# Kernel tuning notes

Measured on AMD Instinct MI355X. Metric: run time of the kernel, lower is better.

Reference implementation:

```python
import jax, jax.numpy as jnp
import numpy as np

N_NODES = 50000
N_EDGES = 800000
NFEAT, NHID, NCLASS = 512, 256, 128
N_UV = 2048


def gcn_layer(x, adj_row, adj_col, adj_val, W, b):
    # support = x @ W ; out = A @ support (sparse COO spmm) + b
    support = x @ W                                   # [N, out]
    msgs = adj_val[:, None] * support[adj_col]        # [E, out]
    out = jax.ops.segment_sum(msgs, adj_row, num_segments=N_NODES)
    return out + b


def setup_inputs() -> dict:
    key = jax.random.key(0)
    ks = jax.random.split(key, 12)
    u = jax.random.randint(ks[0], (N_UV,), 0, N_NODES)
    v = jax.random.randint(ks[1], (N_UV,), 0, N_NODES)
    x = jax.random.normal(ks[2], (N_NODES, NFEAT), dtype=jnp.float32)
    adj_row = jnp.sort(jax.random.randint(ks[3], (N_EDGES,), 0, N_NODES))
    adj_col = jax.random.randint(ks[4], (N_EDGES,), 0, N_NODES)
    adj_val = jax.random.uniform(ks[5], (N_EDGES,), dtype=jnp.float32)
    s1 = 1.0 / np.sqrt(NHID)
    s2 = 1.0 / np.sqrt(NCLASS)
    W1 = jax.random.uniform(ks[6], (NFEAT, NHID), minval=-s1, maxval=s1, dtype=jnp.float32)
    b1 = jax.random.uniform(ks[7], (NHID,), minval=-s1, maxval=s1, dtype=jnp.float32)
    W2 = jax.random.uniform(ks[8], (NHID, NCLASS), minval=-s2, maxval=s2, dtype=jnp.float32)
    b2 = jax.random.uniform(ks[9], (NCLASS,), minval=-s2, maxval=s2, dtype=jnp.float32)
    We = jax.random.normal(ks[10], (NCLASS, NCLASS), dtype=jnp.float32) * (1.0 / np.sqrt(NCLASS))
    return {"u": u, "v": v, "x": x, "adj_row": adj_row, "adj_col": adj_col,
            "adj_val": adj_val, "W1": W1, "b1": b1, "W2": W2, "b2": b2, "We": We}


def reference(u, v, x, adj_row, adj_col, adj_val, W1, b1, W2, b2, We):
    # layer 1: GCN + ReLU (dropout is identity in eval mode)
    h = jax.nn.relu(gcn_layer(x, adj_row, adj_col, adj_val, W1, b1))
    # layer 2: GCN
    z = gcn_layer(h, adj_row, adj_col, adj_val, W2, b2)          # [N, nclass]
    # edge scoring: sigmoid(w_edge(z[u]) @ z[v].T)
    zu = z[u] @ We.T                                             # [U, nclass] (nn.Linear: x @ W.T)
    zv = z[v]                                                    # [V, nclass]
    p_uv = jax.nn.sigmoid(zu @ zv.T)                             # [U, V]
    return p_uv
```

## Files before the change

### kernel.cpp

```cpp
#include <hip/hip_runtime.h>
#include <hip/hip_bf16.h>
#include <math.h>

#define N_NODES 50000
#define N_EDGES 800000
#define NFEAT   512
#define NHID    256
#define NCLASS  128
#define N_UV    2048

#define Q24_SCALE  524288.0f
#define Q24_INV    1.9073486328125e-6f

typedef __bf16    bf16x8 __attribute__((ext_vector_type(8)));
typedef short     s16x8  __attribute__((ext_vector_type(8)));
typedef float     f32x4  __attribute__((ext_vector_type(4)));

struct __attribute__((packed)) U3 { unsigned a, b, c; };

__device__ __forceinline__ unsigned short bf16_rn(float f) {
  unsigned u = __float_as_uint(f);
  u += 0x7fffu + ((u >> 16) & 1u);
  return (unsigned short)(u >> 16);
}
__device__ __forceinline__ float bf16_to_f(unsigned short h) {
  return __uint_as_float(((unsigned)h) << 16);
}
__device__ __forceinline__ void unpack24(unsigned a, unsigned b, unsigned c,
                                         int& e0, int& e1, int& e2, int& e3) {
  e0 = ((int)(a << 8)) >> 8;
  e1 = ((int)((b << 16) | ((a >> 24) << 8))) >> 8;
  e2 = ((int)((c << 24) | ((b >> 16) << 8))) >> 8;
  e3 = ((int)c) >> 8;
}

#define LDSPAD 72

template <bool ASPLIT, int OMODE>
__global__ __launch_bounds__(256, 4) void gemm_mfma_wide(
    const float* __restrict__ Af,
    const unsigned short* __restrict__ Ahi, const unsigned short* __restrict__ Alo,
    const unsigned short* __restrict__ BThi, const unsigned short* __restrict__ BTlo,
    float* __restrict__ C, unsigned char* __restrict__ Cq,
    const float* __restrict__ bias, int M, int N, int K) {
  __shared__ unsigned short sAh[2][64 * LDSPAD];
  __shared__ unsigned short sAl[2][64 * LDSPAD];

  const int tid  = threadIdx.x;
  const int lane = tid & 63;
  const int wave = tid >> 6;
  const int wn   = wave << 5;
  const int lm   = lane & 15;
  const int quad = lane >> 4;
  const int m0   = blockIdx.y * 64;
  const int n0   = blockIdx.x * 128;

  const int r32 = tid >> 4;
  const int c32 = (tid & 15) * 4;
  const int r16 = tid >> 3;
  const int c16 = (tid & 7) * 8;

  float4 pA[4]; s16x8 pAh[2], pAl[2];

  f32x4 acc[4][2];
#pragma unroll
  for (int i = 0; i < 4; ++i)
#pragma unroll
    for (int j = 0; j < 2; ++j)
#pragma unroll
      for (int r = 0; r < 4; ++r) acc[i][j][r] = 0.f;

#define LOAD_TILE(k0)                                                          \
  do {                                                                         \
    if (ASPLIT) {                                                              \
      _Pragma("unroll") for (int p = 0; p < 4; ++p) {                          \
        const int m = m0 + p * 16 + r32;                                       \
        pA[p] = make_float4(0.f, 0.f, 0.f, 0.f);                               \
        if (m < M) pA[p] = *(const float4*)&Af[(size_t)m * K + (k0) + c32];    \
      }                                                                        \
    } else {                                                                   \
      _Pragma("unroll") for (int p = 0; p < 2; ++p) {                          \
        const int m = m0 + p * 32 + r16;                                       \
        _Pragma("unroll") for (int e = 0; e < 8; ++e) { pAh[p][e] = 0; pAl[p][e] = 0; } \
        if (m < M) {                                                           \
          pAh[p] = *(const s16x8*)&Ahi[(size_t)m * K + (k0) + c16];            \
          pAl[p] = *(const s16x8*)&Alo[(size_t)m * K + (k0) + c16];            \
        }                                                                      \
      }                                                                        \
    }                                                                          \
  } while (0)

#define SPLIT4W(v, hv, lv)                                                     \
  hv.x = bf16_rn(v.x); lv.x = bf16_rn(v.x - bf16_to_f(hv.x));                  \
  hv.y = bf16_rn(v.y); lv.y = bf16_rn(v.y - bf16_to_f(hv.y));                  \
  hv.z = bf16_rn(v.z); lv.z = bf16_rn(v.z - bf16_to_f(hv.z));                  \
  hv.w = bf16_rn(v.w); lv.w = bf16_rn(v.w - bf16_to_f(hv.w));

#define STORE_TILE(buf)                                                        \
  do {                                                                         \
    if (ASPLIT) {                                                              \
      _Pragma("unroll") for (int p = 0; p < 4; ++p) {                          \
        ushort4 hv, lv; SPLIT4W(pA[p], hv, lv);                                \
        const int row = p * 16 + r32;                                          \
        *(ushort4*)&sAh[buf][row * LDSPAD + c32] = hv;                         \
        *(ushort4*)&sAl[buf][row * LDSPAD + c32] = lv;                         \
      }                                                                        \
    } else {                                                                   \
      _Pragma("unroll") for (int p = 0; p < 2; ++p) {                          \
        const int row = p * 32 + r16;                                          \
        *(s16x8*)&sAh[buf][row * LDSPAD + c16] = pAh[p];                       \
        *(s16x8*)&sAl[buf][row * LDSPAD + c16] = pAl[p];                       \
      }                                                                        \
    }                                                                          \
  } while (0)

  LOAD_TILE(0);
  STORE_TILE(0);

  const unsigned short* Bhrow = BThi + (size_t)(n0 + wn + lm) * K;
  const unsigned short* Blrow = BTlo + (size_t)(n0 + wn + lm) * K;

  __syncthreads();

  const int NT = K >> 6;
  for (int t = 0; t < NT; ++t) {
    const int k0  = t << 6;
    const int cur = t & 1;
    const unsigned short* bufh = &sAh[cur][0];
    const unsigned short* bufl = &sAl[cur][0];

    bf16x8 bH[2][2], bL[2][2];
#pragma unroll
    for (int ks = 0; ks < 2; ++ks)
#pragma unroll
      for (int j = 0; j < 2; ++j) {
        const size_t off = (size_t)(j * 16) * K + k0 + ks * 32 + quad * 8;
        bH[ks][j] = __builtin_bit_cast(bf16x8, *(const s16x8*)(Bhrow + off));
        bL[ks][j] = __builtin_bit_cast(bf16x8, *(const s16x8*)(Blrow + off));
      }

    if (t + 1 < NT) LOAD_TILE(k0 + 64);

#pragma unroll
    for (int ks = 0; ks < 2; ++ks) {
      const int koff = ks * 32 + quad * 8;
#pragma unroll
      for (int i = 0; i < 4; ++i) {
        const int r = i * 16 + lm;
        const bf16x8 aH = __builtin_bit_cast(bf16x8, *(const s16x8*)&bufh[r * LDSPAD + koff]);
        const bf16x8 aL = __builtin_bit_cast(bf16x8, *(const s16x8*)&bufl[r * LDSPAD + koff]);
#pragma unroll
        for (int j = 0; j < 2; ++j) {
          acc[i][j] = __builtin_amdgcn_mfma_f32_16x16x32_bf16(aH, bH[ks][j], acc[i][j], 0, 0, 0);
          acc[i][j] = __builtin_amdgcn_mfma_f32_16x16x32_bf16(aH, bL[ks][j], acc[i][j], 0, 0, 0);
          acc[i][j] = __builtin_amdgcn_mfma_f32_16x16x32_bf16(aL, bH[ks][j], acc[i][j], 0, 0, 0);
        }
      }
    }

    if (t + 1 < NT) STORE_TILE(cur ^ 1);
    __syncthreads();
  }

#pragma unroll
  for (int i = 0; i < 4; ++i)
#pragma unroll
    for (int j = 0; j < 2; ++j) {
      const int col = n0 + wn + j * 16 + lm;
      const float bb = (OMODE == 3) ? bias[col] : 0.f;
#pragma unroll
      for (int r = 0; r < 4; ++r) {
        const int row = m0 + i * 16 + quad * 4 + r;
        if (row < M) {
          float v = acc[i][j][r];
          if (OMODE == 2) {
            int q = __float2int_rn(v * Q24_SCALE);
            q = q > 8388607 ? 8388607 : (q < -8388608 ? -8388608 : q);
            unsigned char* p = Cq + ((size_t)row * N + col) * 3;
            p[0] = (unsigned char)(q & 0xFF);
            p[1] = (unsigned char)((q >> 8) & 0xFF);
            p[2] = (unsigned char)((q >> 16) & 0xFF);
          } else if (OMODE == 3) {
            C[(size_t)row * N + col] = v + bb;
          } else {
            C[(size_t)row * N + col] = v;
          }
        }
      }
    }
#undef LOAD_TILE
#undef STORE_TILE
#undef SPLIT4W
}

template <int OMODE>
__global__ __launch_bounds__(256, 2) void gemm_mfma_split(
    const float* __restrict__ Af, const float* __restrict__ BTf,
    float* __restrict__ C, int M, int N, int K) {
  __shared__ unsigned short sAh[128 * LDSPAD];
  __shared__ unsigned short sAl[128 * LDSPAD];
  __shared__ unsigned short sBh[128 * LDSPAD];
  __shared__ unsigned short sBl[128 * LDSPAD];

  const int tid  = threadIdx.x;
  const int lane = tid & 63;
  const int wave = tid >> 6;
  const int wm   = (wave >> 1) << 6;
  const int wn   = (wave & 1) << 6;
  const int lm   = lane & 15;
  const int quad = lane >> 4;
  const int m0   = blockIdx.y * 128;
  const int n0   = blockIdx.x * 128;

  const int r32 = tid >> 4;
  const int c32 = (tid & 15) * 4;

  float4 pA[8];
  float4 pB[8];

  f32x4 acc[4][4];
#pragma unroll
  for (int i = 0; i < 4; ++i)
#pragma unroll
    for (int j = 0; j < 4; ++j)
#pragma unroll
      for (int r = 0; r < 4; ++r) acc[i][j][r] = 0.f;

#define LOAD_TILE(k0)                                                          \
  do {                                                                         \
    _Pragma("unroll") for (int p = 0; p < 8; ++p) {                            \
      const int m = m0 + p * 16 + r32;                                         \
      pA[p] = make_float4(0.f, 0.f, 0.f, 0.f);                                 \
      if (m < M) pA[p] = *(const float4*)&Af[(size_t)m * K + (k0) + c32];      \
    }                                                                          \
    _Pragma("unroll") for (int p = 0; p < 8; ++p) {                            \
      const int n = n0 + p * 16 + r32;                                         \
      pB[p] = *(const float4*)&BTf[(size_t)n * K + (k0) + c32];                \
    }                                                                          \
  } while (0)

#define SPLIT4(v, hv, lv)                                                      \
  hv.x = bf16_rn(v.x); lv.x = bf16_rn(v.x - bf16_to_f(hv.x));                  \
  hv.y = bf16_rn(v.y); lv.y = bf16_rn(v.y - bf16_to_f(hv.y));                  \
  hv.z = bf16_rn(v.z); lv.z = bf16_rn(v.z - bf16_to_f(hv.z));                  \
  hv.w = bf16_rn(v.w); lv.w = bf16_rn(v.w - bf16_to_f(hv.w));

#define STORE_TILE()                                                           \
  do {                                                                         \
    _Pragma("unroll") for (int p = 0; p < 8; ++p) {                            \
      ushort4 hv, lv; SPLIT4(pA[p], hv, lv);                                   \
      const int row = p * 16 + r32;                                            \
      *(ushort4*)&sAh[row * LDSPAD + c32] = hv;                                \
      *(ushort4*)&sAl[row * LDSPAD + c32] = lv;                                \
    }                                                                          \
    _Pragma("unroll") for (int p = 0; p < 8; ++p) {                            \
      ushort4 hv, lv; SPLIT4(pB[p], hv, lv);                                   \
      const int row = p * 16 + r32;                                            \
      *(ushort4*)&sBh[row * LDSPAD + c32] = hv;                                \
      *(ushort4*)&sBl[row * LDSPAD + c32] = lv;                                \
    }                                                                          \
  } while (0)

  LOAD_TILE(0);

  for (int k0 = 0; k0 < K; k0 += 64) {
    if (k0) __syncthreads();
    STORE_TILE();
    __syncthreads();
    if (k0 + 64 < K) LOAD_TILE(k0 + 64);

#pragma unroll
    for (int ks = 0; ks < 2; ++ks) {
      const int koff = ks * 32 + quad * 8;
      bf16x8 aH[4], aL[4], bH[4], bL[4];
#pragma unroll
      for (int i = 0; i < 4; ++i) {
        const int r = wm + i * 16 + lm;
        aH[i] = __builtin_bit_cast(bf16x8, *(const s16x8*)&sAh[r * LDSPAD + koff]);
        aL[i] = __builtin_bit_cast(bf16x8, *(const s16x8*)&sAl[r * LDSPAD + koff]);
      }
#pragma unroll
      for (int j = 0; j < 4; ++j) {
        const int r = wn + j * 16 + lm;
        bH[j] = __builtin_bit_cast(bf16x8, *(const s16x8*)&sBh[r * LDSPAD + koff]);
        bL[j] = __builtin_bit_cast(bf16x8, *(const s16x8*)&sBl[r * LDSPAD + koff]);
      }
#pragma unroll
      for (int i = 0; i < 4; ++i)
#pragma unroll
        for (int j = 0; j < 4; ++j) {
          acc[i][j] = __builtin_amdgcn_mfma_f32_16x16x32_bf16(aH[i], bH[j], acc[i][j], 0, 0, 0);
          acc[i][j] = __builtin_amdgcn_mfma_f32_16x16x32_bf16(aH[i], bL[j], acc[i][j], 0, 0, 0);
          acc[i][j] = __builtin_amdgcn_mfma_f32_16x16x32_bf16(aL[i], bH[j], acc[i][j], 0, 0, 0);
        }
    }
  }

#pragma unroll
  for (int i = 0; i < 4; ++i)
#pragma unroll
    for (int j = 0; j < 4; ++j) {
      const int col = n0 + wn + j * 16 + lm;
#pragma unroll
      for (int r = 0; r < 4; ++r) {
        const int row = m0 + wm + i * 16 + quad * 4 + r;
        if (row < M) {
          float v = acc[i][j][r];
          if (OMODE == 1) v = 1.f / (1.f + expf(-v));
          C[(size_t)row * N + col] = v;
        }
      }
    }
#undef LOAD_TILE
#undef STORE_TILE
#undef SPLIT4
}

__global__ __launch_bounds__(256) void prep_all(
    const int* __restrict__ rows, int* __restrict__ row_ptr,
    const float* __restrict__ W1, unsigned short* __restrict__ W1Thi,
    unsigned short* __restrict__ W1Tlo,
    const float* __restrict__ W2, unsigned short* __restrict__ W2Thi,
    unsigned short* __restrict__ W2Tlo) {
  const int idx = blockIdx.x * 256 + threadIdx.x;
  if (idx < N_EDGES) {
    const int r = rows[idx];
    const int rprev = (idx == 0) ? -1 : rows[idx - 1];
    for (int n = rprev + 1; n <= r; ++n) row_ptr[n] = idx;
    if (idx == N_EDGES - 1)
      for (int n = r + 1; n <= N_NODES; ++n) row_ptr[n] = N_EDGES;
  }
  if (idx < NFEAT * NHID) {
    const int n = idx / NFEAT;
    const int k = idx - n * NFEAT;
    const float f = W1[(size_t)k * NHID + n];
    const unsigned short h = bf16_rn(f);
    W1Thi[idx] = h;
    W1Tlo[idx] = bf16_rn(f - bf16_to_f(h));
  }
  if (idx < NHID * NCLASS) {
    const int n = idx / NHID;
    const int k = idx - n * NHID;
    const float f = W2[(size_t)k * NCLASS + n];
    const unsigned short h = bf16_rn(f);
    W2Thi[idx] = h;
    W2Tlo[idx] = bf16_rn(f - bf16_to_f(h));
  }
}

__global__ __launch_bounds__(256, 4) void spmm256_q24_f32(
    const unsigned char* __restrict__ Sq, const int* __restrict__ row_ptr,
    const int* __restrict__ cols, const float* __restrict__ vals,
    const float4* __restrict__ bias4, float4* __restrict__ outF) {
  const int wave = threadIdx.x >> 6;
  const int lane = threadIdx.x & 63;
  const int node = blockIdx.x * 4 + wave;

  const int lou = __builtin_amdgcn_readfirstlane(row_ptr[node]);
  const int hiu = __builtin_amdgcn_readfirstlane(row_ptr[node + 1]);

  float4 acc = make_float4(0.f, 0.f, 0.f, 0.f);
  const int lane12 = lane * 12;

  for (int base = lou; base < hiu; base += 16) {
    int   c[16];
    float w[16];
    if (base + 16 <= hiu) {
#pragma unroll
      for (int t = 0; t < 16; ++t) {
        c[t] = cols[base + t];
        w[t] = vals[base + t] * Q24_INV;
      }
    } else {
#pragma unroll
      for (int t = 0; t < 16; ++t) {
        const int idx = base + t;
        const int ide = idx < hiu ? idx : hiu - 1;
        c[t] = cols[ide];
        w[t] = idx < hiu ? vals[ide] * Q24_INV : 0.f;
      }
    }
    U3 d[16];
#pragma unroll
    for (int t = 0; t < 16; ++t)
      d[t] = *(const U3*)&Sq[(size_t)c[t] * (NHID * 3) + lane12];
#pragma unroll
    for (int t = 0; t < 16; ++t) {
      int e0, e1, e2, e3;
      unpack24(d[t].a, d[t].b, d[t].c, e0, e1, e2, e3);
      acc.x = fmaf(w[t], (float)e0, acc.x);
      acc.y = fmaf(w[t], (float)e1, acc.y);
      acc.z = fmaf(w[t], (float)e2, acc.z);
      acc.w = fmaf(w[t], (float)e3, acc.w);
    }
  }

  const float4 b = bias4[lane];
  acc.x = fmaxf(acc.x + b.x, 0.f);
  acc.y = fmaxf(acc.y + b.y, 0.f);
  acc.z = fmaxf(acc.z + b.z, 0.f);
  acc.w = fmaxf(acc.w + b.w, 0.f);

  outF[(size_t)node * 64 + lane] = acc;
}

__global__ __launch_bounds__(256, 4) void spmm256_f32_list(
    const float4* __restrict__ H4, const int* __restrict__ row_ptr,
    const int* __restrict__ cols, const float* __restrict__ vals,
    const int* __restrict__ u, const int* __restrict__ v,
    float4* __restrict__ out4) {
  const int wave = threadIdx.x >> 6;
  const int lane = threadIdx.x & 63;
  const int idx  = blockIdx.x * 4 + wave;
  const int node = idx < N_UV ? u[idx] : v[idx - N_UV];

  const int lou = __builtin_amdgcn_readfirstlane(row_ptr[node]);
  const int hiu = __builtin_amdgcn_readfirstlane(row_ptr[node + 1]);

  float4 acc = make_float4(0.f, 0.f, 0.f, 0.f);

  for (int base = lou; base < hiu; base += 16) {
    int   c[16];
    float w[16];
    if (base + 16 <= hiu) {
#pragma unroll
      for (int t = 0; t < 16; ++t) { c[t] = cols[base + t]; w[t] = vals[base + t]; }
    } else {
#pragma unroll
      for (int t = 0; t < 16; ++t) {
        const int e = base + t;
        const int ie = e < hiu ? e : hiu - 1;
        c[t] = cols[ie];
        w[t] = e < hiu ? vals[ie] : 0.f;
      }
    }
    float4 r[16];
#pragma unroll
    for (int t = 0; t < 16; ++t) r[t] = H4[(size_t)c[t] * 64 + lane];
#pragma unroll
    for (int t = 0; t < 16; ++t) {
      acc.x = fmaf(w[t], r[t].x, acc.x); acc.y = fmaf(w[t], r[t].y, acc.y);
      acc.z = fmaf(w[t], r[t].z, acc.z); acc.w = fmaf(w[t], r[t].w, acc.w);
    }
  }

  out4[(size_t)idx * 64 + lane] = acc;
}

extern "C" void kernel_launch(void* const* d_in, const int* in_sizes, int n_in,
                              void* d_out, int out_size, void* d_ws, size_t ws_size,
                              hipStream_t stream) {
  const int*   u       = (const int*)  d_in[0];
  const int*   v       = (const int*)  d_in[1];
  const float* x       = (const float*)d_in[2];
  const int*   adj_row = (const int*)  d_in[3];
  const int*   adj_col = (const int*)  d_in[4];
  const float* adj_val = (const float*)d_in[5];
  const float* W1      = (const float*)d_in[6];
  const float* b1      = (const float*)d_in[7];
  const float* W2      = (const float*)d_in[8];
  const float* b2      = (const float*)d_in[9];
  const float* We      = (const float*)d_in[10];
  float* out = (float*)d_out;

  char* wsb = (char*)d_ws;
  unsigned char* S1q = (unsigned char*)wsb;
  float* ZUV2 = (float*)wsb;
  float* ZUV  = (float*)(wsb + (4u << 20));
  float* ZU   = (float*)(wsb + (6u << 20));
  float* Hf = (float*)(wsb + (size_t)N_NODES * NHID * sizeof(float));
  unsigned short* W1Thi = (unsigned short*)out;
  unsigned short* W1Tlo = W1Thi + NHID * NFEAT;
  unsigned short* W2Thi = W1Tlo + NHID * NFEAT;
  unsigned short* W2Tlo = W2Thi + NCLASS * NHID;
  int* row_ptr = (int*)(W2Tlo + NCLASS * NHID);

  prep_all<<<(N_EDGES + 255) / 256, 256, 0, stream>>>(
      adj_row, row_ptr, W1, W1Thi, W1Tlo, W2, W2Thi, W2Tlo);

  gemm_mfma_wide<true, 2>
      <<<dim3(NHID / 128, (N_NODES + 63) / 64), 256, 0, stream>>>(
      x, nullptr, nullptr, W1Thi, W1Tlo,
      nullptr, S1q, nullptr, N_NODES, NHID, NFEAT);

  spmm256_q24_f32<<<N_NODES / 4, 256, 0, stream>>>(
      S1q, row_ptr, adj_col, adj_val, (const float4*)b1, (float4*)Hf);

  spmm256_f32_list<<<(2 * N_UV) / 4, 256, 0, stream>>>(
      (const float4*)Hf, row_ptr, adj_col, adj_val, u, v, (float4*)ZUV2);

  gemm_mfma_wide<true, 3>
      <<<dim3(NCLASS / 128, (2 * N_UV) / 64), 256, 0, stream>>>(
      ZUV2, nullptr, nullptr, W2Thi, W2Tlo,
      ZUV, nullptr, b2, 2 * N_UV, NCLASS, NHID);

  gemm_mfma_split<0>
      <<<dim3(NCLASS / 128, N_UV / 128), 256, 0, stream>>>(
      ZUV, We, ZU, N_UV, NCLASS, NCLASS);

  gemm_mfma_split<1>
      <<<dim3(N_UV / 128, N_UV / 128), 256, 0, stream>>>(
      ZU, ZUV + (size_t)N_UV * NCLASS, out, N_UV, N_UV, NCLASS);
}
```

Baseline: 365.2 us.

## Fold edge weight We into W2 and pre-split zv to drop two GEMM launches

Precomputes W2·We^T and b2·We^T in a small prep kernel, so the u-half of the layer-2 GEMM directly yields z[u]@We^T while the v-half uses plain W2. The v-half output is written pre-split into bf16 hi/lo, which lets the final scoring GEMM reuse the wide kernel with sigmoid epilogue instead of the split-on-the-fly kernel. This removes the separate We GEMM and the in-loop conversion of B in the final GEMM. It adds a prep launch and changes the rounding order of the We product, which slightly alters numerics.

```diff
diff --git a/kernel.cpp b/kernel.cpp
--- a/kernel.cpp
+++ b/kernel.cpp
@@ -41,8 +41,11 @@
     const float* __restrict__ Af,
     const unsigned short* __restrict__ Ahi, const unsigned short* __restrict__ Alo,
     const unsigned short* __restrict__ BThi, const unsigned short* __restrict__ BTlo,
+    const unsigned short* __restrict__ BThi2, const unsigned short* __restrict__ BTlo2,
     float* __restrict__ C, unsigned char* __restrict__ Cq,
-    const float* __restrict__ bias, int M, int N, int K) {
+    unsigned short* __restrict__ Chi, unsigned short* __restrict__ Clo,
+    const float* __restrict__ bias, const float* __restrict__ bias2,
+    int M, int N, int K) {
   __shared__ unsigned short sAh[2][64 * LDSPAD];
   __shared__ unsigned short sAl[2][64 * LDSPAD];
 
@@ -54,6 +57,11 @@
   const int quad = lane >> 4;
   const int m0   = blockIdx.y * 64;
   const int n0   = blockIdx.x * 128;
+
+  const bool vh = (OMODE == 5) && ((int)blockIdx.y >= (M >> 7));
+  const unsigned short* selBh = (OMODE == 5 && vh) ? BThi2 : BThi;
+  const unsigned short* selBl = (OMODE == 5 && vh) ? BTlo2 : BTlo;
+  const float*          selBi = (OMODE == 5 && vh) ? bias2 : bias;
 
   const int r32 = tid >> 4;
   const int c32 = (tid & 15) * 4;
@@ -117,8 +125,8 @@
   LOAD_TILE(0);
   STORE_TILE(0);
 
-  const unsigned short* Bhrow = BThi + (size_t)(n0 + wn + lm) * K;
-  const unsigned short* Blrow = BTlo + (size_t)(n0 + wn + lm) * K;
+  const unsigned short* Bhrow = selBh + (size_t)(n0 + wn + lm) * K;
+  const unsigned short* Blrow = selBl + (size_t)(n0 + wn + lm) * K;
 
   __syncthreads();
 
@@ -167,7 +175,7 @@
 #pragma unroll
     for (int j = 0; j < 2; ++j) {
       const int col = n0 + wn + j * 16 + lm;
-      const float bb = (OMODE == 3) ? bias[col] : 0.f;
+      const float bb = (OMODE == 3 || OMODE == 5) ? selBi[col] : 0.f;
 #pragma unroll
       for (int r = 0; r < 4; ++r) {
         const int row = m0 + i * 16 + quad * 4 + r;
@@ -180,8 +188,20 @@
             p[0] = (unsigned char)(q & 0xFF);
             p[1] = (unsigned char)((q >> 8) & 0xFF);
             p[2] = (unsigned char)((q >> 16) & 0xFF);
+          } else if (OMODE == 1) {
+            C[(size_t)row * N + col] = 1.f / (1.f + expf(-v));
           } else if (OMODE == 3) {
             C[(size_t)row * N + col] = v + bb;
+          } else if (OMODE == 5) {
+            v += bb;
+            if (!vh) {
+              C[(size_t)row * N + col] = v;
+            } else {
+              const unsigned short h = bf16_rn(v);
+              const size_t o = (size_t)(row - (M >> 1)) * N + col;
+              Chi[o] = h;
+              Clo[o] = bf16_rn(v - bf16_to_f(h));
+            }
           } else {
             C[(size_t)row * N + col] = v;
           }
@@ -191,129 +211,6 @@
 #undef LOAD_TILE
 #undef STORE_TILE
 #undef SPLIT4W
-}
-
-template <int OMODE>
-__global__ __launch_bounds__(256, 2) void gemm_mfma_split(
-    const float* __restrict__ Af, const float* __restrict__ BTf,
-    float* __restrict__ C, int M, int N, int K) {
-  __shared__ unsigned short sAh[128 * LDSPAD];
-  __shared__ unsigned short sAl[128 * LDSPAD];
-  __shared__ unsigned short sBh[128 * LDSPAD];
-  __shared__ unsigned short sBl[128 * LDSPAD];
-
-  const int tid  = threadIdx.x;
-  const int lane = tid & 63;
-  const int wave = tid >> 6;
-  const int wm   = (wave >> 1) << 6;
-  const int wn   = (wave & 1) << 6;
-  const int lm   = lane & 15;
-  const int quad = lane >> 4;
-  const int m0   = blockIdx.y * 128;
-  const int n0   = blockIdx.x * 128;
-
-  const int r32 = tid >> 4;
-  const int c32 = (tid & 15) * 4;
-
-  float4 pA[8];
-  float4 pB[8];
-
-  f32x4 acc[4][4];
-#pragma unroll
-  for (int i = 0; i < 4; ++i)
-#pragma unroll
-    for (int j = 0; j < 4; ++j)
-#pragma unroll
-      for (int r = 0; r < 4; ++r) acc[i][j][r] = 0.f;
-
-#define LOAD_TILE(k0)                                                          \
-  do {                                                                         \
-    _Pragma("unroll") for (int p = 0; p < 8; ++p) {                            \
-      const int m = m0 + p * 16 + r32;                                         \
-      pA[p] = make_float4(0.f, 0.f, 0.f, 0.f);                                 \
-      if (m < M) pA[p] = *(const float4*)&Af[(size_t)m * K + (k0) + c32];      \
-    }                                                                          \
-    _Pragma("unroll") for (int p = 0; p < 8; ++p) {                            \
-      const int n = n0 + p * 16 + r32;                                         \
-      pB[p] = *(const float4*)&BTf[(size_t)n * K + (k0) + c32];                \
-    }                                                                          \
-  } while (0)
-
-#define SPLIT4(v, hv, lv)                                                      \
-  hv.x = bf16_rn(v.x); lv.x = bf16_rn(v.x - bf16_to_f(hv.x));                  \
-  hv.y = bf16_rn(v.y); lv.y = bf16_rn(v.y - bf16_to_f(hv.y));                  \
-  hv.z = bf16_rn(v.z); lv.z = bf16_rn(v.z - bf16_to_f(hv.z));                  \
-  hv.w = bf16_rn(v.w); lv.w = bf16_rn(v.w - bf16_to_f(hv.w));
-
-#define STORE_TILE()                                                           \
-  do {                                                                         \
-    _Pragma("unroll") for (int p = 0; p < 8; ++p) {                            \
-      ushort4 hv, lv; SPLIT4(pA[p], hv, lv);                                   \
-      const int row = p * 16 + r32;                                            \
-      *(ushort4*)&sAh[row * LDSPAD + c32] = hv;                                \
-      *(ushort4*)&sAl[row * LDSPAD + c32] = lv;                                \
-    }                                                                          \
-    _Pragma("unroll") for (int p = 0; p < 8; ++p) {                            \
-      ushort4 hv, lv; SPLIT4(pB[p], hv, lv);                                   \
-      const int row = p * 16 + r32;                                            \
-      *(ushort4*)&sBh[row * LDSPAD + c32] = hv;                                \
-      *(ushort4*)&sBl[row * LDSPAD + c32] = lv;                                \
-    }                                                                          \
-  } while (0)
-
-  LOAD_TILE(0);
-
-  for (int k0 = 0; k0 < K; k0 += 64) {
-    if (k0) __syncthreads();
-    STORE_TILE();
-    __syncthreads();
-    if (k0 + 64 < K) LOAD_TILE(k0 + 64);
-
-#pragma unroll
-    for (int ks = 0; ks < 2; ++ks) {
-      const int koff = ks * 32 + quad * 8;
-      bf16x8 aH[4], aL[4], bH[4], bL[4];
-#pragma unroll
-      for (int i = 0; i < 4; ++i) {
-        const int r = wm + i * 16 + lm;
-        aH[i] = __builtin_bit_cast(bf16x8, *(const s16x8*)&sAh[r * LDSPAD + koff]);
-        aL[i] = __builtin_bit_cast(bf16x8, *(const s16x8*)&sAl[r * LDSPAD + koff]);
-      }
-#pragma unroll
-      for (int j = 0; j < 4; ++j) {
-        const int r = wn + j * 16 + lm;
-        bH[j] = __builtin_bit_cast(bf16x8, *(const s16x8*)&sBh[r * LDSPAD + koff]);
-        bL[j] = __builtin_bit_cast(bf16x8, *(const s16x8*)&sBl[r * LDSPAD + koff]);
-      }
-#pragma unroll
-      for (int i = 0; i < 4; ++i)
-#pragma unroll
-        for (int j = 0; j < 4; ++j) {
-          acc[i][j] = __builtin_amdgcn_mfma_f32_16x16x32_bf16(aH[i], bH[j], acc[i][j], 0, 0, 0);
-          acc[i][j] = __builtin_amdgcn_mfma_f32_16x16x32_bf16(aH[i], bL[j], acc[i][j], 0, 0, 0);
-          acc[i][j] = __builtin_amdgcn_mfma_f32_16x16x32_bf16(aL[i], bH[j], acc[i][j], 0, 0, 0);
-        }
-    }
-  }
-
-#pragma unroll
-  for (int i = 0; i < 4; ++i)
-#pragma unroll
-    for (int j = 0; j < 4; ++j) {
-      const int col = n0 + wn + j * 16 + lm;
-#pragma unroll
-      for (int r = 0; r < 4; ++r) {
-        const int row = m0 + wm + i * 16 + quad * 4 + r;
-        if (row < M) {
-          float v = acc[i][j][r];
-          if (OMODE == 1) v = 1.f / (1.f + expf(-v));
-          C[(size_t)row * N + col] = v;
-        }
-      }
-    }
-#undef LOAD_TILE
-#undef STORE_TILE
-#undef SPLIT4
 }
 
 __global__ __launch_bounds__(256) void prep_all(
@@ -345,6 +242,40 @@
     const unsigned short h = bf16_rn(f);
     W2Thi[idx] = h;
     W2Tlo[idx] = bf16_rn(f - bf16_to_f(h));
+  }
+}
+
+__global__ __launch_bounds__(256) void prep_w2e(
+    const float* __restrict__ W2, const float* __restrict__ We,
+    const float* __restrict__ b2,
+    unsigned short* __restrict__ W2eThi, unsigned short* __restrict__ W2eTlo,
+    float* __restrict__ b2e) {
+  const int idx = blockIdx.x * 256 + threadIdx.x;
+  const int n = idx >> 8;
+  const int k = idx & 255;
+  const float4* wr = (const float4*)(We + (size_t)n * NCLASS);
+  const float4* ar = (const float4*)(W2 + (size_t)k * NCLASS);
+  float s = 0.f;
+#pragma unroll
+  for (int c = 0; c < NCLASS / 4; ++c) {
+    const float4 a = ar[c], w = wr[c];
+    s = fmaf(a.x, w.x, s); s = fmaf(a.y, w.y, s);
+    s = fmaf(a.z, w.z, s); s = fmaf(a.w, w.w, s);
+  }
+  const unsigned short h = bf16_rn(s);
+  W2eThi[idx] = h;
+  W2eTlo[idx] = bf16_rn(s - bf16_to_f(h));
+  if (idx < NCLASS) {
+    const float4* br = (const float4*)b2;
+    const float4* w2 = (const float4*)(We + (size_t)idx * NCLASS);
+    float t = 0.f;
+#pragma unroll
+    for (int c = 0; c < NCLASS / 4; ++c) {
+      const float4 a = br[c], w = w2[c];
+      t = fmaf(a.x, w.x, t); t = fmaf(a.y, w.y, t);
+      t = fmaf(a.z, w.z, t); t = fmaf(a.w, w.w, t);
+    }
+    b2e[idx] = t;
   }
 }
 
@@ -466,22 +397,28 @@
   char* wsb = (char*)d_ws;
   unsigned char* S1q = (unsigned char*)wsb;
   float* ZUV2 = (float*)wsb;
-  float* ZUV  = (float*)(wsb + (4u << 20));
-  float* ZU   = (float*)(wsb + (6u << 20));
+  float* ZU   = (float*)(wsb + (4u << 20));
+  unsigned short* ZVhi = (unsigned short*)(wsb + (5u << 20));
+  unsigned short* ZVlo = (unsigned short*)(wsb + (5u << 20) + (512u << 10));
   float* Hf = (float*)(wsb + (size_t)N_NODES * NHID * sizeof(float));
   unsigned short* W1Thi = (unsigned short*)out;
   unsigned short* W1Tlo = W1Thi + NHID * NFEAT;
   unsigned short* W2Thi = W1Tlo + NHID * NFEAT;
   unsigned short* W2Tlo = W2Thi + NCLASS * NHID;
   int* row_ptr = (int*)(W2Tlo + NCLASS * NHID);
+  unsigned short* W2eThi = (unsigned short*)(row_ptr + N_NODES + 4);
+  unsigned short* W2eTlo = W2eThi + NCLASS * NHID;
+  float* b2e = (float*)(W2eTlo + NCLASS * NHID);
 
   prep_all<<<(N_EDGES + 255) / 256, 256, 0, stream>>>(
       adj_row, row_ptr, W1, W1Thi, W1Tlo, W2, W2Thi, W2Tlo);
+  prep_w2e<<<(NCLASS * NHID) / 256, 256, 0, stream>>>(
+      W2, We, b2, W2eThi, W2eTlo, b2e);
 
   gemm_mfma_wide<true, 2>
       <<<dim3(NHID / 128, (N_NODES + 63) / 64), 256, 0, stream>>>(
-      x, nullptr, nullptr, W1Thi, W1Tlo,
-      nullptr, S1q, nullptr, N_NODES, NHID, NFEAT);
+      x, nullptr, nullptr, W1Thi, W1Tlo, nullptr, nullptr,
+      nullptr, S1q, nullptr, nullptr, nullptr, nullptr, N_NODES, NHID, NFEAT);
 
   spmm256_q24_f32<<<N_NODES / 4, 256, 0, stream>>>(
       S1q, row_ptr, adj_col, adj_val, (const float4*)b1, (float4*)Hf);
@@ -489,16 +426,13 @@
   spmm256_f32_list<<<(2 * N_UV) / 4, 256, 0, stream>>>(
       (const float4*)Hf, row_ptr, adj_col, adj_val, u, v, (float4*)ZUV2);
 
-  gemm_mfma_wide<true, 3>
+  gemm_mfma_wide<true, 5>
       <<<dim3(NCLASS / 128, (2 * N_UV) / 64), 256, 0, stream>>>(
-      ZUV2, nullptr, nullptr, W2Thi, W2Tlo,
-      ZUV, nullptr, b2, 2 * N_UV, NCLASS, NHID);
-
-  gemm_mfma_split<0>
-      <<<dim3(NCLASS / 128, N_UV / 128), 256, 0, stream>>>(
-      ZUV, We, ZU, N_UV, NCLASS, NCLASS);
-
-  gemm_mfma_split<1>
-      <<<dim3(N_UV / 128, N_UV / 128), 256, 0, stream>>>(
-      ZU, ZUV + (size_t)N_UV * NCLASS, out, N_UV, N_UV, NCLASS);
-}
+      ZUV2, nullptr, nullptr, W2eThi, W2eTlo, W2Thi, W2Tlo,
+      ZU, nullptr, ZVhi, ZVlo, b2e, b2, 2 * N_UV, NCLASS, NHID);
+
+  gemm_mfma_wide<true, 1>
+      <<<dim3(N_UV / 128, N_UV / 64), 256, 0, stream>>>(
+      ZU, nullptr, nullptr, ZVhi, ZVlo, nullptr, nullptr,
+      out, nullptr, nullptr, nullptr, nullptr, nullptr, N_UV, N_UV, NCLASS);
+}
```

Result: no change. 364.6 us (-0.2%).
